# Performance work log

Hardware: AMD Instinct MI355X
Metric: run time of the kernel (lower is better)

## Reference

```python
import jax, jax.numpy as jnp
import numpy as np

B, S, HID, NH, HD = 2, 2048, 1024, 16, 64


def setup_inputs() -> dict:
    key = jax.random.key(0)
    k0, k1, k2, k3 = jax.random.split(key, 4)
    scale = 1.0 / np.sqrt(HID)
    return {
        "x": jax.random.normal(k0, (B, S, HID), dtype=jnp.float32),
        "wq": jax.random.normal(k1, (HID, HID), dtype=jnp.float32) * scale,
        "wk": jax.random.normal(k2, (HID, HID), dtype=jnp.float32) * scale,
        "wv": jax.random.normal(k3, (HID, HID), dtype=jnp.float32) * scale,
    }


def reference(x, wq, wk, wv):
    b, s, _ = x.shape
    # nn.Linear(bias=False): y = x @ W^T ; reshape to [B, H, S, D]
    q = (x @ wq.T).reshape(b, s, NH, HD).transpose(0, 2, 1, 3)
    k = (x @ wk.T).reshape(b, s, NH, HD).transpose(0, 2, 1, 3)
    v = (x @ wv.T).reshape(b, s, NH, HD).transpose(0, 2, 1, 3)
    att = jnp.einsum("bhqd,bhkd->bhqk", q, k) / np.sqrt(HD)
    score = jax.nn.softmax(att.astype(jnp.float32), axis=-1)  # dropout p=0.0 -> identity
    attv = jnp.einsum("bhqk,bhkd->bhqd", score, v)  # [B, H, S, D]
    # faithful to original bug: .view(B, S, -1) on contiguous [B,H,S,D] WITHOUT transpose back
    attv = attv.reshape(b, s, NH * HD)
    return score, attv
```

## Files before the change

### kernel.cpp

```cpp
#include <hip/hip_runtime.h>
#include <hip/hip_bf16.h>
#include <stdint.h>
#include <stddef.h>

#define NB 2
#define SEQ 2048
#define HIDN 1024
#define NHEAD 16
#define HDIM 64
#define MTOT (NB * SEQ)

typedef short bf16x8 __attribute__((ext_vector_type(8)));
typedef _Float16 f16x8 __attribute__((ext_vector_type(8)));
typedef __fp16 h16x2 __attribute__((ext_vector_type(2)));
typedef float f32x4 __attribute__((ext_vector_type(4)));
typedef uint32_t u32x4 __attribute__((ext_vector_type(4)));

#define MFMA16(a, b, c)  __builtin_amdgcn_mfma_f32_16x16x32_bf16(a, b, c, 0, 0, 0)
#define MFMAH16(a, b, c) __builtin_amdgcn_mfma_f32_16x16x32_f16(a, b, c, 0, 0, 0)

__device__ __forceinline__ unsigned short f2bf(float f) {
  union { float f; uint32_t u; } v; v.f = f;
  uint32_t u = v.u;
  uint32_t r = (u + 0x7fffu + ((u >> 16) & 1u)) >> 16;
  return (unsigned short)r;
}

__device__ __forceinline__ unsigned short f2h(float f) {
  _Float16 h = (_Float16)f;
  return *reinterpret_cast<unsigned short*>(&h);
}

__device__ __forceinline__ float h2f(unsigned short u) {
  _Float16 h = *reinterpret_cast<_Float16*>(&u);
  return (float)h;
}

__device__ __forceinline__ void gload16(const void* g, void* l) {
  __builtin_amdgcn_global_load_lds((const __attribute__((address_space(1))) void*)g,
                                   (__attribute__((address_space(3))) void*)l,
                                   16, 0, 0);
}

__global__ void cvt_bf16(const float* __restrict__ x, const float* __restrict__ wq,
                         const float* __restrict__ wk, const float* __restrict__ wv,
                         unsigned short* __restrict__ dst)
{
  size_t i4 = ((size_t)blockIdx.x * blockDim.x + threadIdx.x) * 4;
  const float* s; size_t off;
  if (i4 < 4194304UL)      { s = x;  off = i4; }
  else if (i4 < 5242880UL) { s = wq; off = i4 - 4194304UL; }
  else if (i4 < 6291456UL) { s = wk; off = i4 - 5242880UL; }
  else                     { s = wv; off = i4 - 6291456UL; }
  float4 v = *(const float4*)(s + off);
  ushort4 o;
  o.x = f2bf(v.x); o.y = f2bf(v.y); o.z = f2bf(v.z); o.w = f2bf(v.w);
  *(ushort4*)(dst + i4) = o;
}

__global__ __launch_bounds__(256, 2) void qkv_gemm(
    const unsigned short* __restrict__ xb,
    const unsigned short* __restrict__ wqb,
    const unsigned short* __restrict__ wkb,
    const unsigned short* __restrict__ wvb,
    unsigned short* __restrict__ Qb,
    unsigned short* __restrict__ Kb,
    unsigned short* __restrict__ Vt)
{
  __shared__ unsigned short As[128 * 64];
  __shared__ unsigned short Bs[128 * 64];

  const int z = blockIdx.z;
  const unsigned short* W = (z == 0) ? wqb : (z == 1) ? wkb : wvb;
  const int n0 = blockIdx.x * 128;
  const int m0 = blockIdx.y * 128;
  const int tid = threadIdx.x;
  const int lane = tid & 63;
  const int wid = tid >> 6;
  const int l15 = lane & 15;
  const int lg = lane >> 4;

  f32x4 acc[4][4] = {};

  const int wr = (wid >> 1) * 64;
  const int wc = (wid & 1) * 64;

  for (int kt = 0; kt < 16; ++kt) {
    __syncthreads();
    #pragma unroll
    for (int i = 0; i < 4; ++i) {
      int row = wid * 32 + i * 8 + (lane >> 3);
      int chunk = (lane & 7) ^ (row & 7);
      const unsigned short* ga = xb + (size_t)(m0 + row) * HIDN + kt * 64 + chunk * 8;
      const unsigned short* gb = W  + (size_t)(n0 + row) * HIDN + kt * 64 + chunk * 8;
      gload16(ga, (char*)As + wid * 4096 + i * 1024);
      gload16(gb, (char*)Bs + wid * 4096 + i * 1024);
    }
    __syncthreads();

    #pragma unroll
    for (int ks = 0; ks < 2; ++ks) {
      bf16x8 af[4], bfr[4];
      #pragma unroll
      for (int mi = 0; mi < 4; ++mi) {
        int row = wr + mi * 16 + l15;
        int cb = (ks * 64 + lg * 16) ^ ((row & 7) << 4);
        af[mi] = *(const bf16x8*)((const char*)As + row * 128 + cb);
      }
      #pragma unroll
      for (int ni = 0; ni < 4; ++ni) {
        int row = wc + ni * 16 + l15;
        int cb = (ks * 64 + lg * 16) ^ ((row & 7) << 4);
        bfr[ni] = *(const bf16x8*)((const char*)Bs + row * 128 + cb);
      }
      #pragma unroll
      for (int mi = 0; mi < 4; ++mi)
        #pragma unroll
        for (int ni = 0; ni < 4; ++ni)
          acc[mi][ni] = MFMA16(af[mi], bfr[ni], acc[mi][ni]);
    }
  }

  if (z < 2) {
    unsigned short* O = (z == 0) ? Qb : Kb;
    #pragma unroll
    for (int mi = 0; mi < 4; ++mi)
      #pragma unroll
      for (int ni = 0; ni < 4; ++ni) {
        int n = n0 + wc + ni * 16 + l15;
        #pragma unroll
        for (int e = 0; e < 4; ++e) {
          int m = m0 + wr + mi * 16 + lg * 4 + e;
          if (z == 0) {
            O[(size_t)m * HIDN + n] = f2bf(acc[mi][ni][e]);
          } else {
            int mm = (m & ~31) | (((m >> 2) & 1) << 4) | (((m >> 3) & 3) << 2) | (m & 3);
            int nn = (n & ~56) | (((((n >> 3) & 7) ^ (mm & 7))) << 3);
            O[(size_t)mm * HIDN + nn] = f2bf(acc[mi][ni][e]);
          }
        }
      }
  } else {
    #pragma unroll
    for (int mi = 0; mi < 4; ++mi)
      #pragma unroll
      for (int ni = 0; ni < 4; ++ni) {
        int n = n0 + wc + ni * 16 + l15;
        int m = m0 + wr + mi * 16 + lg * 4;
        int mmv = (m & ~120) | (((((m >> 3) & 15) ^ (n & 15))) << 3);
        ushort4 pk;
        pk.x = f2h(acc[mi][ni][0]);
        pk.y = f2h(acc[mi][ni][1]);
        pk.z = f2h(acc[mi][ni][2]);
        pk.w = f2h(acc[mi][ni][3]);
        *(ushort4*)(Vt + (size_t)n * MTOT + mmv) = pk;
      }
  }
}

__global__ __launch_bounds__(512, 4) void attn_pv(
    const unsigned short* __restrict__ Qb,
    const unsigned short* __restrict__ Kb,
    const unsigned short* __restrict__ Vt,
    float* __restrict__ invs,
    float* __restrict__ out)
{
  __shared__ unsigned short Ks[2][128 * 64];
  __shared__ unsigned short Vs[2][64 * 128];

  const int bid = blockIdx.x;
  const int xcd = bid & 7;
  const int rest = bid >> 3;
  const int pan = (rest & 3) * 8 + xcd;
  const int slab = rest >> 2;
  const int b = pan >> 4, h = pan & 15;
  const int tid = threadIdx.x;
  const int wid = tid >> 6;
  const int lane = tid & 63;
  const int l15 = lane & 15, lg = lane >> 4;
  const int q0 = slab * 128 + wid * 16;

  const unsigned short* qptr = Qb + ((size_t)(b * SEQ + q0 + l15) * HIDN + h * HDIM + lg * 8);
  const bf16x8 bq0 = *(const bf16x8*)qptr;
  const bf16x8 bq1 = *(const bf16x8*)(qptr + 32);

  const float C = 0.18033688011112042f;

  const unsigned short* kpanel = Kb + (size_t)b * SEQ * HIDN + h * HDIM;
  const unsigned short* vpanel = Vt + (size_t)h * HDIM * MTOT + b * SEQ;

  #define STAGE_K(buf, c) { \
    _Pragma("unroll") \
    for (int i = 0; i < 2; ++i) { \
      int row = wid * 8 + i * 64 + (lane >> 3); \
      const unsigned short* src = kpanel + (size_t)((c) * 128 + row) * HIDN + (lane & 7) * 8; \
      gload16(src, (char*)Ks[buf] + wid * 1024 + i * 8192); \
    } }
  #define STAGE_V(buf, c) { \
    _Pragma("unroll") \
    for (int i = 0; i < 2; ++i) { \
      int dl = wid * 4 + i * 32 + (lane >> 4); \
      const unsigned short* src = vpanel + (size_t)dl * MTOT + (c) * 128 + (lane & 15) * 8; \
      gload16(src, (char*)Vs[buf] + wid * 1024 + i * 8192); \
    } }

  STAGE_K(0, 0); STAGE_V(0, 0);
  __builtin_amdgcn_sched_barrier(0);
  asm volatile("s_waitcnt vmcnt(0)" ::: "memory");
  __builtin_amdgcn_s_barrier();
  __builtin_amdgcn_sched_barrier(0);

  float sm = 0.f;
  f32x4 pv[4] = {};

  for (int c = 0; c < 16; ++c) {
    const int cur = c & 1;
    if (c < 15) { STAGE_K(cur ^ 1, c + 1); STAGE_V(cur ^ 1, c + 1); }
    __builtin_amdgcn_sched_barrier(0);

    f32x4 acc[8] = {};
    #pragma unroll
    for (int kf = 0; kf < 8; ++kf) {
      const int rowL = kf * 16 + l15;
      const char* kr = (const char*)Ks[cur] + rowL * 128;
      bf16x8 a0 = *(const bf16x8*)(kr + ((lg    ) ^ (rowL & 7)) * 16);
      bf16x8 a1 = *(const bf16x8*)(kr + ((lg + 4) ^ (rowL & 7)) * 16);
      acc[kf] = MFMA16(a0, bq0, acc[kf]);
      acc[kf] = MFMA16(a1, bq1, acc[kf]);
    }

    #pragma unroll
    for (int t = 0; t < 4; ++t) {
      float4 s0, s1;
      s0.x = exp2f(acc[2 * t][0] * C);
      s0.y = exp2f(acc[2 * t][1] * C);
      s0.z = exp2f(acc[2 * t][2] * C);
      s0.w = exp2f(acc[2 * t][3] * C);
      s1.x = exp2f(acc[2 * t + 1][0] * C);
      s1.y = exp2f(acc[2 * t + 1][1] * C);
      s1.z = exp2f(acc[2 * t + 1][2] * C);
      s1.w = exp2f(acc[2 * t + 1][3] * C);
      sm += ((s0.x + s0.y) + (s0.z + s0.w)) + ((s1.x + s1.y) + (s1.z + s1.w));

      union PKu { h16x2 h2[4]; f16x8 h8; } pk;
      pk.h2[0] = __builtin_amdgcn_cvt_pkrtz(s0.x, s0.y);
      pk.h2[1] = __builtin_amdgcn_cvt_pkrtz(s0.z, s0.w);
      pk.h2[2] = __builtin_amdgcn_cvt_pkrtz(s1.x, s1.y);
      pk.h2[3] = __builtin_amdgcn_cvt_pkrtz(s1.z, s1.w);

      #pragma unroll
      for (int nf = 0; nf < 4; ++nf) {
        const int d = nf * 16 + l15;
        f16x8 bv = *(const f16x8*)((const char*)Vs[cur] + d * 256 + (((t * 4 + lg) ^ l15)) * 16);
        pv[nf] = MFMAH16(pk.h8, bv, pv[nf]);
      }
    }

    __builtin_amdgcn_sched_barrier(0);
    asm volatile("s_waitcnt vmcnt(0)" ::: "memory");
    __builtin_amdgcn_s_barrier();
    __builtin_amdgcn_sched_barrier(0);
  }

  #pragma unroll
  for (int off = 16; off <= 32; off <<= 1) sm += __shfl_xor(sm, off, 64);
  const float inv = __builtin_amdgcn_rcpf(sm);
  if (lane < 16) invs[(size_t)(b * NHEAD + h) * SEQ + q0 + lane] = inv;

  float* av = out + (size_t)NB * NHEAD * SEQ * SEQ
            + ((size_t)(b * NHEAD + h) * SEQ + q0 + 4 * lg) * HDIM + l15;
  #pragma unroll
  for (int e = 0; e < 4; ++e) {
    const float invq = __shfl(inv, 4 * lg + e, 64);
    #pragma unroll
    for (int nf = 0; nf < 4; ++nf)
      __builtin_nontemporal_store(pv[nf][e] * invq, av + (size_t)e * HDIM + nf * 16);
  }
  #undef STAGE_K
  #undef STAGE_V
}

__global__ __launch_bounds__(512, 2) void score_emit(
    const unsigned short* __restrict__ Qb,
    const unsigned short* __restrict__ Kb,
    const float* __restrict__ invs,
    float* __restrict__ out)
{
  __shared__ unsigned short P[16 * 2048];

  const int bid = blockIdx.x;
  const int xcd = bid & 7;
  const int rest = bid >> 3;
  const int pan = (rest & 3) * 8 + xcd;
  const int blkp = rest >> 2;
  const int b = pan >> 4, h = pan & 15;
  const int tid = threadIdx.x;
  const int wid = tid >> 6;
  const int lane = tid & 63;
  const int l15 = lane & 15, lg = lane >> 4;

  const float C = 0.18033688011112042f;
  const unsigned short* kpanel = Kb + (size_t)b * SEQ * HIDN + h * HDIM;
  const size_t panrow0 = (size_t)(b * NHEAD + h) * SEQ;

  for (int tt = 0; tt < 8; ++tt) {
    const int q0 = (blkp * 8 + tt) * 16;

    const unsigned short* qptr = Qb + ((size_t)(b * SEQ + q0 + l15) * HIDN + h * HDIM + lg * 8);
    const bf16x8 bq0 = *(const bf16x8*)qptr;
    const bf16x8 bq1 = *(const bf16x8*)(qptr + 32);

    #pragma unroll
    for (int i = 0; i < 2; ++i) {
      const int c = wid * 2 + i;
      f32x4 acc[8] = {};
      #pragma unroll
      for (int kf = 0; kf < 8; ++kf) {
        const int s = c * 128 + kf * 16 + l15;
        const unsigned short* kr = kpanel + (size_t)s * HIDN;
        bf16x8 a0 = *(const bf16x8*)(kr + ((lg      ^ (s & 7))) * 8);
        bf16x8 a1 = *(const bf16x8*)(kr + (((lg + 4) ^ (s & 7))) * 8);
        acc[kf] = MFMA16(a0, bq0, acc[kf]);
        acc[kf] = MFMA16(a1, bq1, acc[kf]);
      }
      #pragma unroll
      for (int t = 0; t < 4; ++t) {
        float4 s0, s1;
        s0.x = exp2f(acc[2 * t][0] * C);
        s0.y = exp2f(acc[2 * t][1] * C);
        s0.z = exp2f(acc[2 * t][2] * C);
        s0.w = exp2f(acc[2 * t][3] * C);
        s1.x = exp2f(acc[2 * t + 1][0] * C);
        s1.y = exp2f(acc[2 * t + 1][1] * C);
        s1.z = exp2f(acc[2 * t + 1][2] * C);
        s1.w = exp2f(acc[2 * t + 1][3] * C);

        union PKu { h16x2 h2[4]; u32x4 u4; } pk;
        pk.h2[0] = __builtin_amdgcn_cvt_pkrtz(s0.x, s0.y);
        pk.h2[1] = __builtin_amdgcn_cvt_pkrtz(s0.z, s0.w);
        pk.h2[2] = __builtin_amdgcn_cvt_pkrtz(s1.x, s1.y);
        pk.h2[3] = __builtin_amdgcn_cvt_pkrtz(s1.z, s1.w);

        const int off = c * 256 + ((((t * 4 + lg) ^ l15)) << 4);
        *(u32x4*)((char*)P + l15 * 4096 + off) = pk.u4;
      }
    }

    asm volatile("s_waitcnt lgkmcnt(0)" ::: "memory");
    __builtin_amdgcn_s_barrier();
    __builtin_amdgcn_sched_barrier(0);

    #pragma unroll
    for (int i = 0; i < 2; ++i) {
      const int r = wid * 2 + i;
      const float invr = invs[panrow0 + q0 + r];
      float* orow = out + (panrow0 + q0 + r) * SEQ;
      #pragma unroll
      for (int g = 0; g < 8; ++g) {
        const int o = g * 512 + lane * 8;
        const int ph = o ^ ((r & 15) << 4);
        uint2 w = *(const uint2*)((const char*)P + r * 4096 + ph);
        f32x4 ov;
        ov[0] = h2f((unsigned short)(w.x & 0xffff)) * invr;
        ov[1] = h2f((unsigned short)(w.x >> 16)) * invr;
        ov[2] = h2f((unsigned short)(w.y & 0xffff)) * invr;
        ov[3] = h2f((unsigned short)(w.y >> 16)) * invr;
        __builtin_nontemporal_store(ov, (f32x4*)(orow + (o >> 1)));
      }
    }

    asm volatile("s_waitcnt lgkmcnt(0)" ::: "memory");
    __builtin_amdgcn_s_barrier();
    __builtin_amdgcn_sched_barrier(0);
  }
}

extern "C" void kernel_launch(void* const* d_in, const int* in_sizes, int n_in,
                              void* d_out, int out_size, void* d_ws, size_t ws_size,
                              hipStream_t stream)
{
  const float* x  = (const float*)d_in[0];
  const float* wq = (const float*)d_in[1];
  const float* wk = (const float*)d_in[2];
  const float* wv = (const float*)d_in[3];
  float* out = (float*)d_out;
  unsigned short* ws = (unsigned short*)d_ws;

  unsigned short* xb  = ws;
  unsigned short* wqb = ws + 4194304;
  unsigned short* wkb = ws + 5242880;
  unsigned short* wvb = ws + 6291456;
  unsigned short* Qb  = ws + 7340032;
  unsigned short* Kb  = ws + 11534336;
  unsigned short* Vt  = ws + 15728640;
  float* invs = (float*)ws;

  cvt_bf16<<<7168, 256, 0, stream>>>(x, wq, wk, wv, ws);
  qkv_gemm<<<dim3(8, 32, 3), 256, 0, stream>>>(xb, wqb, wkb, wvb, Qb, Kb, Vt);
  attn_pv<<<512, 512, 0, stream>>>(Qb, Kb, Vt, invs, out);
  score_emit<<<512, 512, 0, stream>>>(Qb, Kb, invs, out);
}
```

Baseline: 195.0 us.

## Fuse PV attention and score emission into one kernel with per-tile row sums

Merges the two attention kernels into one. Each 16-row query tile computes QK^T exp values across all keys split over 8 waves, and reduces row sums through shared memory. It then writes normalized scores and computes P·V from register-held fp16 probabilities, followed by a cross-wave reduction of partial outputs in LDS. This removes the second QK^T recompute, the extra kernel launch and the invs round trip. In exchange it adds extra barriers, loads V directly from global without LDS staging, and adds an LDS reduction per tile.

```diff
diff --git a/kernel.cpp b/kernel.cpp
--- a/kernel.cpp
+++ b/kernel.cpp
@@ -158,135 +158,14 @@
   }
 }
 
-__global__ __launch_bounds__(512, 4) void attn_pv(
+__global__ __launch_bounds__(512, 2) void attn_all(
     const unsigned short* __restrict__ Qb,
     const unsigned short* __restrict__ Kb,
     const unsigned short* __restrict__ Vt,
-    float* __restrict__ invs,
-    float* __restrict__ out)
-{
-  __shared__ unsigned short Ks[2][128 * 64];
-  __shared__ unsigned short Vs[2][64 * 128];
-
-  const int bid = blockIdx.x;
-  const int xcd = bid & 7;
-  const int rest = bid >> 3;
-  const int pan = (rest & 3) * 8 + xcd;
-  const int slab = rest >> 2;
-  const int b = pan >> 4, h = pan & 15;
-  const int tid = threadIdx.x;
-  const int wid = tid >> 6;
-  const int lane = tid & 63;
-  const int l15 = lane & 15, lg = lane >> 4;
-  const int q0 = slab * 128 + wid * 16;
-
-  const unsigned short* qptr = Qb + ((size_t)(b * SEQ + q0 + l15) * HIDN + h * HDIM + lg * 8);
-  const bf16x8 bq0 = *(const bf16x8*)qptr;
-  const bf16x8 bq1 = *(const bf16x8*)(qptr + 32);
-
-  const float C = 0.18033688011112042f;
-
-  const unsigned short* kpanel = Kb + (size_t)b * SEQ * HIDN + h * HDIM;
-  const unsigned short* vpanel = Vt + (size_t)h * HDIM * MTOT + b * SEQ;
-
-  #define STAGE_K(buf, c) { \
-    _Pragma("unroll") \
-    for (int i = 0; i < 2; ++i) { \
-      int row = wid * 8 + i * 64 + (lane >> 3); \
-      const unsigned short* src = kpanel + (size_t)((c) * 128 + row) * HIDN + (lane & 7) * 8; \
-      gload16(src, (char*)Ks[buf] + wid * 1024 + i * 8192); \
-    } }
-  #define STAGE_V(buf, c) { \
-    _Pragma("unroll") \
-    for (int i = 0; i < 2; ++i) { \
-      int dl = wid * 4 + i * 32 + (lane >> 4); \
-      const unsigned short* src = vpanel + (size_t)dl * MTOT + (c) * 128 + (lane & 15) * 8; \
-      gload16(src, (char*)Vs[buf] + wid * 1024 + i * 8192); \
-    } }
-
-  STAGE_K(0, 0); STAGE_V(0, 0);
-  __builtin_amdgcn_sched_barrier(0);
-  asm volatile("s_waitcnt vmcnt(0)" ::: "memory");
-  __builtin_amdgcn_s_barrier();
-  __builtin_amdgcn_sched_barrier(0);
-
-  float sm = 0.f;
-  f32x4 pv[4] = {};
-
-  for (int c = 0; c < 16; ++c) {
-    const int cur = c & 1;
-    if (c < 15) { STAGE_K(cur ^ 1, c + 1); STAGE_V(cur ^ 1, c + 1); }
-    __builtin_amdgcn_sched_barrier(0);
-
-    f32x4 acc[8] = {};
-    #pragma unroll
-    for (int kf = 0; kf < 8; ++kf) {
-      const int rowL = kf * 16 + l15;
-      const char* kr = (const char*)Ks[cur] + rowL * 128;
-      bf16x8 a0 = *(const bf16x8*)(kr + ((lg    ) ^ (rowL & 7)) * 16);
-      bf16x8 a1 = *(const bf16x8*)(kr + ((lg + 4) ^ (rowL & 7)) * 16);
-      acc[kf] = MFMA16(a0, bq0, acc[kf]);
-      acc[kf] = MFMA16(a1, bq1, acc[kf]);
-    }
-
-    #pragma unroll
-    for (int t = 0; t < 4; ++t) {
-      float4 s0, s1;
-      s0.x = exp2f(acc[2 * t][0] * C);
-      s0.y = exp2f(acc[2 * t][1] * C);
-      s0.z = exp2f(acc[2 * t][2] * C);
-      s0.w = exp2f(acc[2 * t][3] * C);
-      s1.x = exp2f(acc[2 * t + 1][0] * C);
-      s1.y = exp2f(acc[2 * t + 1][1] * C);
-      s1.z = exp2f(acc[2 * t + 1][2] * C);
-      s1.w = exp2f(acc[2 * t + 1][3] * C);
-      sm += ((s0.x + s0.y) + (s0.z + s0.w)) + ((s1.x + s1.y) + (s1.z + s1.w));
-
-      union PKu { h16x2 h2[4]; f16x8 h8; } pk;
-      pk.h2[0] = __builtin_amdgcn_cvt_pkrtz(s0.x, s0.y);
-      pk.h2[1] = __builtin_amdgcn_cvt_pkrtz(s0.z, s0.w);
-      pk.h2[2] = __builtin_amdgcn_cvt_pkrtz(s1.x, s1.y);
-      pk.h2[3] = __builtin_amdgcn_cvt_pkrtz(s1.z, s1.w);
-
-      #pragma unroll
-      for (int nf = 0; nf < 4; ++nf) {
-        const int d = nf * 16 + l15;
-        f16x8 bv = *(const f16x8*)((const char*)Vs[cur] + d * 256 + (((t * 4 + lg) ^ l15)) * 16);
-        pv[nf] = MFMAH16(pk.h8, bv, pv[nf]);
-      }
-    }
-
-    __builtin_amdgcn_sched_barrier(0);
-    asm volatile("s_waitcnt vmcnt(0)" ::: "memory");
-    __builtin_amdgcn_s_barrier();
-    __builtin_amdgcn_sched_barrier(0);
-  }
-
-  #pragma unroll
-  for (int off = 16; off <= 32; off <<= 1) sm += __shfl_xor(sm, off, 64);
-  const float inv = __builtin_amdgcn_rcpf(sm);
-  if (lane < 16) invs[(size_t)(b * NHEAD + h) * SEQ + q0 + lane] = inv;
-
-  float* av = out + (size_t)NB * NHEAD * SEQ * SEQ
-            + ((size_t)(b * NHEAD + h) * SEQ + q0 + 4 * lg) * HDIM + l15;
-  #pragma unroll
-  for (int e = 0; e < 4; ++e) {
-    const float invq = __shfl(inv, 4 * lg + e, 64);
-    #pragma unroll
-    for (int nf = 0; nf < 4; ++nf)
-      __builtin_nontemporal_store(pv[nf][e] * invq, av + (size_t)e * HDIM + nf * 16);
-  }
-  #undef STAGE_K
-  #undef STAGE_V
-}
-
-__global__ __launch_bounds__(512, 2) void score_emit(
-    const unsigned short* __restrict__ Qb,
-    const unsigned short* __restrict__ Kb,
-    const float* __restrict__ invs,
     float* __restrict__ out)
 {
   __shared__ unsigned short P[16 * 2048];
+  __shared__ float sums[8][16];
 
   const int bid = blockIdx.x;
   const int xcd = bid & 7;
@@ -301,14 +180,20 @@
 
   const float C = 0.18033688011112042f;
   const unsigned short* kpanel = Kb + (size_t)b * SEQ * HIDN + h * HDIM;
+  const unsigned short* vpanel = Vt + (size_t)h * HDIM * MTOT + b * SEQ;
   const size_t panrow0 = (size_t)(b * NHEAD + h) * SEQ;
+  float* avbase = out + (size_t)NB * NHEAD * SEQ * SEQ;
 
   for (int tt = 0; tt < 8; ++tt) {
-    const int q0 = (blkp * 8 + tt) * 16;
+    const int q0 = blkp * 128 + tt * 16;
 
     const unsigned short* qptr = Qb + ((size_t)(b * SEQ + q0 + l15) * HIDN + h * HDIM + lg * 8);
     const bf16x8 bq0 = *(const bf16x8*)qptr;
     const bf16x8 bq1 = *(const bf16x8*)(qptr + 32);
+
+    union PKu { h16x2 h2[4]; f16x8 h8; u32x4 u4; };
+    u32x4 pkreg[2][4];
+    float sm = 0.f;
 
     #pragma unroll
     for (int i = 0; i < 2; ++i) {
@@ -334,39 +219,92 @@
         s1.y = exp2f(acc[2 * t + 1][1] * C);
         s1.z = exp2f(acc[2 * t + 1][2] * C);
         s1.w = exp2f(acc[2 * t + 1][3] * C);
-
-        union PKu { h16x2 h2[4]; u32x4 u4; } pk;
+        sm += ((s0.x + s0.y) + (s0.z + s0.w)) + ((s1.x + s1.y) + (s1.z + s1.w));
+
+        PKu pk;
         pk.h2[0] = __builtin_amdgcn_cvt_pkrtz(s0.x, s0.y);
         pk.h2[1] = __builtin_amdgcn_cvt_pkrtz(s0.z, s0.w);
         pk.h2[2] = __builtin_amdgcn_cvt_pkrtz(s1.x, s1.y);
         pk.h2[3] = __builtin_amdgcn_cvt_pkrtz(s1.z, s1.w);
+        pkreg[i][t] = pk.u4;
 
         const int off = c * 256 + ((((t * 4 + lg) ^ l15)) << 4);
         *(u32x4*)((char*)P + l15 * 4096 + off) = pk.u4;
       }
     }
+    sm += __shfl_xor(sm, 16, 64);
+    sm += __shfl_xor(sm, 32, 64);
+    if (lane < 16) sums[wid][lane] = sm;
 
     asm volatile("s_waitcnt lgkmcnt(0)" ::: "memory");
     __builtin_amdgcn_s_barrier();
     __builtin_amdgcn_sched_barrier(0);
 
+    float tot = 0.f;
+    #pragma unroll
+    for (int w2 = 0; w2 < 8; ++w2) tot += sums[w2][l15];
+    const float inv = __builtin_amdgcn_rcpf(tot);
+
+    f32x4 pv[4] = {};
+    #pragma unroll
+    for (int i = 0; i < 2; ++i) {
+      const int c = wid * 2 + i;
+      #pragma unroll
+      for (int t = 0; t < 4; ++t) {
+        PKu pk; pk.u4 = pkreg[i][t];
+        #pragma unroll
+        for (int nf = 0; nf < 4; ++nf) {
+          const unsigned short* vp = vpanel + (size_t)(nf * 16 + l15) * MTOT
+                                   + c * 128 + (((t * 4 + lg) ^ l15)) * 8;
+          f16x8 bv = *(const f16x8*)vp;
+          pv[nf] = MFMAH16(pk.h8, bv, pv[nf]);
+        }
+      }
+    }
+
     #pragma unroll
     for (int i = 0; i < 2; ++i) {
       const int r = wid * 2 + i;
-      const float invr = invs[panrow0 + q0 + r];
+      const float invr = __shfl(inv, r, 64);
       float* orow = out + (panrow0 + q0 + r) * SEQ;
       #pragma unroll
       for (int g = 0; g < 8; ++g) {
         const int o = g * 512 + lane * 8;
         const int ph = o ^ ((r & 15) << 4);
-        uint2 w = *(const uint2*)((const char*)P + r * 4096 + ph);
+        uint2 w2 = *(const uint2*)((const char*)P + r * 4096 + ph);
         f32x4 ov;
-        ov[0] = h2f((unsigned short)(w.x & 0xffff)) * invr;
-        ov[1] = h2f((unsigned short)(w.x >> 16)) * invr;
-        ov[2] = h2f((unsigned short)(w.y & 0xffff)) * invr;
-        ov[3] = h2f((unsigned short)(w.y >> 16)) * invr;
+        ov[0] = h2f((unsigned short)(w2.x & 0xffff)) * invr;
+        ov[1] = h2f((unsigned short)(w2.x >> 16)) * invr;
+        ov[2] = h2f((unsigned short)(w2.y & 0xffff)) * invr;
+        ov[3] = h2f((unsigned short)(w2.y >> 16)) * invr;
         __builtin_nontemporal_store(ov, (f32x4*)(orow + (o >> 1)));
       }
+    }
+
+    asm volatile("s_waitcnt lgkmcnt(0)" ::: "memory");
+    __builtin_amdgcn_s_barrier();
+    __builtin_amdgcn_sched_barrier(0);
+
+    float* pvred = (float*)P;
+    #pragma unroll
+    for (int nf = 0; nf < 4; ++nf)
+      #pragma unroll
+      for (int e = 0; e < 4; ++e)
+        pvred[(wid * 16 + (4 * lg + e)) * 68 + nf * 16 + l15] = pv[nf][e];
+
+    asm volatile("s_waitcnt lgkmcnt(0)" ::: "memory");
+    __builtin_amdgcn_s_barrier();
+    __builtin_amdgcn_sched_barrier(0);
+
+    #pragma unroll
+    for (int i = 0; i < 2; ++i) {
+      const int r = wid * 2 + i;
+      const float invr = __shfl(inv, r, 64);
+      float v = 0.f;
+      #pragma unroll
+      for (int w2 = 0; w2 < 8; ++w2)
+        v += pvred[(w2 * 16 + r) * 68 + lane];
+      __builtin_nontemporal_store(v * invr, avbase + (panrow0 + q0 + r) * HDIM + lane);
     }
 
     asm volatile("s_waitcnt lgkmcnt(0)" ::: "memory");
@@ -393,10 +331,8 @@
   unsigned short* Qb  = ws + 7340032;
   unsigned short* Kb  = ws + 11534336;
   unsigned short* Vt  = ws + 15728640;
-  float* invs = (float*)ws;
 
   cvt_bf16<<<7168, 256, 0, stream>>>(x, wq, wk, wv, ws);
   qkv_gemm<<<dim3(8, 32, 3), 256, 0, stream>>>(xb, wqb, wkb, wvb, Qb, Kb, Vt);
-  attn_pv<<<512, 512, 0, stream>>>(Qb, Kb, Vt, invs, out);
-  score_emit<<<512, 512, 0, stream>>>(Qb, Kb, invs, out);
-}
+  attn_all<<<512, 512, 0, stream>>>(Qb, Kb, Vt, out);
+}
```

Result: slower. 238.7 us (+22.4%).

## Double-buffer QKV GEMM LDS tiles and single-buffer K in attention for occupancy

Applied to the files above, without the earlier changes.

The QKV GEMM moves from a sync-load-sync loop to double-buffered LDS. The next k-tile's global-to-LDS copy is issued before computing on the current tile, so load latency overlaps MFMA work. The attention kernel drops K's second LDS buffer, adds a mid-iteration barrier so the next K chunk is loaded only after QK^T finishes, and raises the launch-bounds occupancy hint from 4 to 6. The trade is less LDS per block and more resident blocks, against an extra barrier and less overlap for K loads.

```diff
diff --git a/kernel.cpp b/kernel.cpp
--- a/kernel.cpp
+++ b/kernel.cpp
@@ -67,8 +67,8 @@
     unsigned short* __restrict__ Kb,
     unsigned short* __restrict__ Vt)
 {
-  __shared__ unsigned short As[128 * 64];
-  __shared__ unsigned short Bs[128 * 64];
+  __shared__ unsigned short As[2][128 * 64];
+  __shared__ unsigned short Bs[2][128 * 64];
 
   const int z = blockIdx.z;
   const unsigned short* W = (z == 0) ? wqb : (z == 1) ? wkb : wvb;
@@ -85,18 +85,27 @@
   const int wr = (wid >> 1) * 64;
   const int wc = (wid & 1) * 64;
 
+  #define QSTAGE(buf, kt) { \
+    _Pragma("unroll") \
+    for (int i = 0; i < 4; ++i) { \
+      int row = wid * 32 + i * 8 + (lane >> 3); \
+      int chunk = (lane & 7) ^ (row & 7); \
+      const unsigned short* ga = xb + (size_t)(m0 + row) * HIDN + (kt) * 64 + chunk * 8; \
+      const unsigned short* gb = W  + (size_t)(n0 + row) * HIDN + (kt) * 64 + chunk * 8; \
+      gload16(ga, (char*)As[buf] + wid * 4096 + i * 1024); \
+      gload16(gb, (char*)Bs[buf] + wid * 4096 + i * 1024); \
+    } }
+
+  QSTAGE(0, 0)
+  __builtin_amdgcn_sched_barrier(0);
+  asm volatile("s_waitcnt vmcnt(0) lgkmcnt(0)" ::: "memory");
+  __builtin_amdgcn_s_barrier();
+  __builtin_amdgcn_sched_barrier(0);
+
   for (int kt = 0; kt < 16; ++kt) {
-    __syncthreads();
-    #pragma unroll
-    for (int i = 0; i < 4; ++i) {
-      int row = wid * 32 + i * 8 + (lane >> 3);
-      int chunk = (lane & 7) ^ (row & 7);
-      const unsigned short* ga = xb + (size_t)(m0 + row) * HIDN + kt * 64 + chunk * 8;
-      const unsigned short* gb = W  + (size_t)(n0 + row) * HIDN + kt * 64 + chunk * 8;
-      gload16(ga, (char*)As + wid * 4096 + i * 1024);
-      gload16(gb, (char*)Bs + wid * 4096 + i * 1024);
-    }
-    __syncthreads();
+    const int cur = kt & 1;
+    if (kt < 15) QSTAGE(cur ^ 1, kt + 1)
+    __builtin_amdgcn_sched_barrier(0);
 
     #pragma unroll
     for (int ks = 0; ks < 2; ++ks) {
@@ -105,13 +114,13 @@
       for (int mi = 0; mi < 4; ++mi) {
         int row = wr + mi * 16 + l15;
         int cb = (ks * 64 + lg * 16) ^ ((row & 7) << 4);
-        af[mi] = *(const bf16x8*)((const char*)As + row * 128 + cb);
+        af[mi] = *(const bf16x8*)((const char*)As[cur] + row * 128 + cb);
       }
       #pragma unroll
       for (int ni = 0; ni < 4; ++ni) {
         int row = wc + ni * 16 + l15;
         int cb = (ks * 64 + lg * 16) ^ ((row & 7) << 4);
-        bfr[ni] = *(const bf16x8*)((const char*)Bs + row * 128 + cb);
+        bfr[ni] = *(const bf16x8*)((const char*)Bs[cur] + row * 128 + cb);
       }
       #pragma unroll
       for (int mi = 0; mi < 4; ++mi)
@@ -119,7 +128,13 @@
         for (int ni = 0; ni < 4; ++ni)
           acc[mi][ni] = MFMA16(af[mi], bfr[ni], acc[mi][ni]);
     }
+
+    __builtin_amdgcn_sched_barrier(0);
+    asm volatile("s_waitcnt vmcnt(0) lgkmcnt(0)" ::: "memory");
+    __builtin_amdgcn_s_barrier();
+    __builtin_amdgcn_sched_barrier(0);
   }
+  #undef QSTAGE
 
   if (z < 2) {
     unsigned short* O = (z == 0) ? Qb : Kb;
@@ -158,14 +173,14 @@
   }
 }
 
-__global__ __launch_bounds__(512, 4) void attn_pv(
+__global__ __launch_bounds__(512, 6) void attn_pv(
     const unsigned short* __restrict__ Qb,
     const unsigned short* __restrict__ Kb,
     const unsigned short* __restrict__ Vt,
     float* __restrict__ invs,
     float* __restrict__ out)
 {
-  __shared__ unsigned short Ks[2][128 * 64];
+  __shared__ unsigned short Ks[128 * 64];
   __shared__ unsigned short Vs[2][64 * 128];
 
   const int bid = blockIdx.x;
@@ -189,12 +204,12 @@
   const unsigned short* kpanel = Kb + (size_t)b * SEQ * HIDN + h * HDIM;
   const unsigned short* vpanel = Vt + (size_t)h * HDIM * MTOT + b * SEQ;
 
-  #define STAGE_K(buf, c) { \
+  #define STAGE_K(c) { \
     _Pragma("unroll") \
     for (int i = 0; i < 2; ++i) { \
       int row = wid * 8 + i * 64 + (lane >> 3); \
       const unsigned short* src = kpanel + (size_t)((c) * 128 + row) * HIDN + (lane & 7) * 8; \
-      gload16(src, (char*)Ks[buf] + wid * 1024 + i * 8192); \
+      gload16(src, (char*)Ks + wid * 1024 + i * 8192); \
     } }
   #define STAGE_V(buf, c) { \
     _Pragma("unroll") \
@@ -204,9 +219,9 @@
       gload16(src, (char*)Vs[buf] + wid * 1024 + i * 8192); \
     } }
 
-  STAGE_K(0, 0); STAGE_V(0, 0);
+  STAGE_K(0); STAGE_V(0, 0);
   __builtin_amdgcn_sched_barrier(0);
-  asm volatile("s_waitcnt vmcnt(0)" ::: "memory");
+  asm volatile("s_waitcnt vmcnt(0) lgkmcnt(0)" ::: "memory");
   __builtin_amdgcn_s_barrier();
   __builtin_amdgcn_sched_barrier(0);
 
@@ -215,19 +230,25 @@
 
   for (int c = 0; c < 16; ++c) {
     const int cur = c & 1;
-    if (c < 15) { STAGE_K(cur ^ 1, c + 1); STAGE_V(cur ^ 1, c + 1); }
-    __builtin_amdgcn_sched_barrier(0);
 
     f32x4 acc[8] = {};
     #pragma unroll
     for (int kf = 0; kf < 8; ++kf) {
       const int rowL = kf * 16 + l15;
-      const char* kr = (const char*)Ks[cur] + rowL * 128;
+      const char* kr = (const char*)Ks + rowL * 128;
       bf16x8 a0 = *(const bf16x8*)(kr + ((lg    ) ^ (rowL & 7)) * 16);
       bf16x8 a1 = *(const bf16x8*)(kr + ((lg + 4) ^ (rowL & 7)) * 16);
       acc[kf] = MFMA16(a0, bq0, acc[kf]);
       acc[kf] = MFMA16(a1, bq1, acc[kf]);
     }
+
+    __builtin_amdgcn_sched_barrier(0);
+    asm volatile("s_waitcnt lgkmcnt(0)" ::: "memory");
+    __builtin_amdgcn_s_barrier();
+    __builtin_amdgcn_sched_barrier(0);
+
+    if (c < 15) { STAGE_K(c + 1); STAGE_V(cur ^ 1, c + 1); }
+    __builtin_amdgcn_sched_barrier(0);
 
     #pragma unroll
     for (int t = 0; t < 4; ++t) {
@@ -257,7 +278,7 @@
     }
 
     __builtin_amdgcn_sched_barrier(0);
-    asm volatile("s_waitcnt vmcnt(0)" ::: "memory");
+    asm volatile("s_waitcnt vmcnt(0) lgkmcnt(0)" ::: "memory");
     __builtin_amdgcn_s_barrier();
     __builtin_amdgcn_sched_barrier(0);
   }
```

Measured after the change: 210.1 us. 1.08x slower.

## Merge attention-PV and score-emit kernels into one launch with independent row sums

Applied to the files above, without the earlier changes.

Combines the PV-accumulation kernel and the score-writing kernel into a single 1024-block launch. Even blocks do the PV path and odd blocks write the normalized score matrix. The score blocks now compute their own softmax row sums, reduced through shared memory, instead of reading inverse sums produced by the earlier kernel. This removes the dependency between the two kernels, so the compute-heavy PV blocks and the store-heavy score blocks can run concurrently. The cost is that the exp and QK^T work is done twice, and shared memory per block grows to the larger footprint, which may lower occupancy for the PV blocks.

```diff
diff --git a/kernel.cpp b/kernel.cpp
--- a/kernel.cpp
+++ b/kernel.cpp
@@ -158,171 +158,81 @@
   }
 }
 
-__global__ __launch_bounds__(512, 4) void attn_pv(
+__global__ __launch_bounds__(512, 2) void attn_split(
     const unsigned short* __restrict__ Qb,
     const unsigned short* __restrict__ Kb,
     const unsigned short* __restrict__ Vt,
-    float* __restrict__ invs,
     float* __restrict__ out)
 {
-  __shared__ unsigned short Ks[2][128 * 64];
-  __shared__ unsigned short Vs[2][64 * 128];
+  __shared__ char smem[66048];
 
   const int bid = blockIdx.x;
-  const int xcd = bid & 7;
-  const int rest = bid >> 3;
+  const int gg = bid >> 3;
+  const int type = gg & 1;
+  const int s = (bid & 7) | ((gg >> 1) << 3);
+
+  const int xcd = s & 7;
+  const int rest = s >> 3;
   const int pan = (rest & 3) * 8 + xcd;
-  const int slab = rest >> 2;
   const int b = pan >> 4, h = pan & 15;
   const int tid = threadIdx.x;
   const int wid = tid >> 6;
   const int lane = tid & 63;
   const int l15 = lane & 15, lg = lane >> 4;
-  const int q0 = slab * 128 + wid * 16;
-
-  const unsigned short* qptr = Qb + ((size_t)(b * SEQ + q0 + l15) * HIDN + h * HDIM + lg * 8);
-  const bf16x8 bq0 = *(const bf16x8*)qptr;
-  const bf16x8 bq1 = *(const bf16x8*)(qptr + 32);
 
   const float C = 0.18033688011112042f;
-
   const unsigned short* kpanel = Kb + (size_t)b * SEQ * HIDN + h * HDIM;
-  const unsigned short* vpanel = Vt + (size_t)h * HDIM * MTOT + b * SEQ;
-
-  #define STAGE_K(buf, c) { \
-    _Pragma("unroll") \
-    for (int i = 0; i < 2; ++i) { \
-      int row = wid * 8 + i * 64 + (lane >> 3); \
-      const unsigned short* src = kpanel + (size_t)((c) * 128 + row) * HIDN + (lane & 7) * 8; \
-      gload16(src, (char*)Ks[buf] + wid * 1024 + i * 8192); \
-    } }
-  #define STAGE_V(buf, c) { \
-    _Pragma("unroll") \
-    for (int i = 0; i < 2; ++i) { \
-      int dl = wid * 4 + i * 32 + (lane >> 4); \
-      const unsigned short* src = vpanel + (size_t)dl * MTOT + (c) * 128 + (lane & 15) * 8; \
-      gload16(src, (char*)Vs[buf] + wid * 1024 + i * 8192); \
-    } }
-
-  STAGE_K(0, 0); STAGE_V(0, 0);
-  __builtin_amdgcn_sched_barrier(0);
-  asm volatile("s_waitcnt vmcnt(0)" ::: "memory");
-  __builtin_amdgcn_s_barrier();
-  __builtin_amdgcn_sched_barrier(0);
-
-  float sm = 0.f;
-  f32x4 pv[4] = {};
-
-  for (int c = 0; c < 16; ++c) {
-    const int cur = c & 1;
-    if (c < 15) { STAGE_K(cur ^ 1, c + 1); STAGE_V(cur ^ 1, c + 1); }
-    __builtin_amdgcn_sched_barrier(0);
-
-    f32x4 acc[8] = {};
-    #pragma unroll
-    for (int kf = 0; kf < 8; ++kf) {
-      const int rowL = kf * 16 + l15;
-      const char* kr = (const char*)Ks[cur] + rowL * 128;
-      bf16x8 a0 = *(const bf16x8*)(kr + ((lg    ) ^ (rowL & 7)) * 16);
-      bf16x8 a1 = *(const bf16x8*)(kr + ((lg + 4) ^ (rowL & 7)) * 16);
-      acc[kf] = MFMA16(a0, bq0, acc[kf]);
-      acc[kf] = MFMA16(a1, bq1, acc[kf]);
-    }
-
-    #pragma unroll
-    for (int t = 0; t < 4; ++t) {
-      float4 s0, s1;
-      s0.x = exp2f(acc[2 * t][0] * C);
-      s0.y = exp2f(acc[2 * t][1] * C);
-      s0.z = exp2f(acc[2 * t][2] * C);
-      s0.w = exp2f(acc[2 * t][3] * C);
-      s1.x = exp2f(acc[2 * t + 1][0] * C);
-      s1.y = exp2f(acc[2 * t + 1][1] * C);
-      s1.z = exp2f(acc[2 * t + 1][2] * C);
-      s1.w = exp2f(acc[2 * t + 1][3] * C);
-      sm += ((s0.x + s0.y) + (s0.z + s0.w)) + ((s1.x + s1.y) + (s1.z + s1.w));
-
-      union PKu { h16x2 h2[4]; f16x8 h8; } pk;
-      pk.h2[0] = __builtin_amdgcn_cvt_pkrtz(s0.x, s0.y);
-      pk.h2[1] = __builtin_amdgcn_cvt_pkrtz(s0.z, s0.w);
-      pk.h2[2] = __builtin_amdgcn_cvt_pkrtz(s1.x, s1.y);
-      pk.h2[3] = __builtin_amdgcn_cvt_pkrtz(s1.z, s1.w);
-
-      #pragma unroll
-      for (int nf = 0; nf < 4; ++nf) {
-        const int d = nf * 16 + l15;
-        f16x8 bv = *(const f16x8*)((const char*)Vs[cur] + d * 256 + (((t * 4 + lg) ^ l15)) * 16);
-        pv[nf] = MFMAH16(pk.h8, bv, pv[nf]);
-      }
-    }
-
+  const size_t panrow0 = (size_t)(b * NHEAD + h) * SEQ;
+
+  if (type == 0) {
+    const int slab = rest >> 2;
+    const int q0 = slab * 128 + wid * 16;
+
+    const unsigned short* qptr = Qb + ((size_t)(b * SEQ + q0 + l15) * HIDN + h * HDIM + lg * 8);
+    const bf16x8 bq0 = *(const bf16x8*)qptr;
+    const bf16x8 bq1 = *(const bf16x8*)(qptr + 32);
+    const unsigned short* vpanel = Vt + (size_t)h * HDIM * MTOT + b * SEQ;
+
+    #define STAGE_K(buf, c) { \
+      _Pragma("unroll") \
+      for (int i = 0; i < 2; ++i) { \
+        int row = wid * 8 + i * 64 + (lane >> 3); \
+        const unsigned short* src = kpanel + (size_t)((c) * 128 + row) * HIDN + (lane & 7) * 8; \
+        gload16(src, smem + (buf) * 16384 + wid * 1024 + i * 8192); \
+      } }
+    #define STAGE_V(buf, c) { \
+      _Pragma("unroll") \
+      for (int i = 0; i < 2; ++i) { \
+        int dl = wid * 4 + i * 32 + (lane >> 4); \
+        const unsigned short* src = vpanel + (size_t)dl * MTOT + (c) * 128 + (lane & 15) * 8; \
+        gload16(src, smem + 32768 + (buf) * 16384 + wid * 1024 + i * 8192); \
+      } }
+
+    STAGE_K(0, 0); STAGE_V(0, 0);
     __builtin_amdgcn_sched_barrier(0);
     asm volatile("s_waitcnt vmcnt(0)" ::: "memory");
     __builtin_amdgcn_s_barrier();
     __builtin_amdgcn_sched_barrier(0);
-  }
-
-  #pragma unroll
-  for (int off = 16; off <= 32; off <<= 1) sm += __shfl_xor(sm, off, 64);
-  const float inv = __builtin_amdgcn_rcpf(sm);
-  if (lane < 16) invs[(size_t)(b * NHEAD + h) * SEQ + q0 + lane] = inv;
-
-  float* av = out + (size_t)NB * NHEAD * SEQ * SEQ
-            + ((size_t)(b * NHEAD + h) * SEQ + q0 + 4 * lg) * HDIM + l15;
-  #pragma unroll
-  for (int e = 0; e < 4; ++e) {
-    const float invq = __shfl(inv, 4 * lg + e, 64);
-    #pragma unroll
-    for (int nf = 0; nf < 4; ++nf)
-      __builtin_nontemporal_store(pv[nf][e] * invq, av + (size_t)e * HDIM + nf * 16);
-  }
-  #undef STAGE_K
-  #undef STAGE_V
-}
-
-__global__ __launch_bounds__(512, 2) void score_emit(
-    const unsigned short* __restrict__ Qb,
-    const unsigned short* __restrict__ Kb,
-    const float* __restrict__ invs,
-    float* __restrict__ out)
-{
-  __shared__ unsigned short P[16 * 2048];
-
-  const int bid = blockIdx.x;
-  const int xcd = bid & 7;
-  const int rest = bid >> 3;
-  const int pan = (rest & 3) * 8 + xcd;
-  const int blkp = rest >> 2;
-  const int b = pan >> 4, h = pan & 15;
-  const int tid = threadIdx.x;
-  const int wid = tid >> 6;
-  const int lane = tid & 63;
-  const int l15 = lane & 15, lg = lane >> 4;
-
-  const float C = 0.18033688011112042f;
-  const unsigned short* kpanel = Kb + (size_t)b * SEQ * HIDN + h * HDIM;
-  const size_t panrow0 = (size_t)(b * NHEAD + h) * SEQ;
-
-  for (int tt = 0; tt < 8; ++tt) {
-    const int q0 = (blkp * 8 + tt) * 16;
-
-    const unsigned short* qptr = Qb + ((size_t)(b * SEQ + q0 + l15) * HIDN + h * HDIM + lg * 8);
-    const bf16x8 bq0 = *(const bf16x8*)qptr;
-    const bf16x8 bq1 = *(const bf16x8*)(qptr + 32);
-
-    #pragma unroll
-    for (int i = 0; i < 2; ++i) {
-      const int c = wid * 2 + i;
+
+    float sm = 0.f;
+    f32x4 pv[4] = {};
+
+    for (int c = 0; c < 16; ++c) {
+      const int cur = c & 1;
+      if (c < 15) { STAGE_K(cur ^ 1, c + 1); STAGE_V(cur ^ 1, c + 1); }
+      __builtin_amdgcn_sched_barrier(0);
+
       f32x4 acc[8] = {};
       #pragma unroll
       for (int kf = 0; kf < 8; ++kf) {
-        const int s = c * 128 + kf * 16 + l15;
-        const unsigned short* kr = kpanel + (size_t)s * HIDN;
-        bf16x8 a0 = *(const bf16x8*)(kr + ((lg      ^ (s & 7))) * 8);
-        bf16x8 a1 = *(const bf16x8*)(kr + (((lg + 4) ^ (s & 7))) * 8);
+        const int rowL = kf * 16 + l15;
+        const char* kr = smem + cur * 16384 + rowL * 128;
+        bf16x8 a0 = *(const bf16x8*)(kr + ((lg    ) ^ (rowL & 7)) * 16);
+        bf16x8 a1 = *(const bf16x8*)(kr + ((lg + 4) ^ (rowL & 7)) * 16);
         acc[kf] = MFMA16(a0, bq0, acc[kf]);
         acc[kf] = MFMA16(a1, bq1, acc[kf]);
       }
+
       #pragma unroll
       for (int t = 0; t < 4; ++t) {
         float4 s0, s1;
@@ -334,44 +244,129 @@
         s1.y = exp2f(acc[2 * t + 1][1] * C);
         s1.z = exp2f(acc[2 * t + 1][2] * C);
         s1.w = exp2f(acc[2 * t + 1][3] * C);
-
-        union PKu { h16x2 h2[4]; u32x4 u4; } pk;
+        sm += ((s0.x + s0.y) + (s0.z + s0.w)) + ((s1.x + s1.y) + (s1.z + s1.w));
+
+        union PKu { h16x2 h2[4]; f16x8 h8; } pk;
         pk.h2[0] = __builtin_amdgcn_cvt_pkrtz(s0.x, s0.y);
         pk.h2[1] = __builtin_amdgcn_cvt_pkrtz(s0.z, s0.w);
         pk.h2[2] = __builtin_amdgcn_cvt_pkrtz(s1.x, s1.y);
         pk.h2[3] = __builtin_amdgcn_cvt_pkrtz(s1.z, s1.w);
 
-        const int off = c * 256 + ((((t * 4 + lg) ^ l15)) << 4);
-        *(u32x4*)((char*)P + l15 * 4096 + off) = pk.u4;
-      }
-    }
-
-    asm volatile("s_waitcnt lgkmcnt(0)" ::: "memory");
-    __builtin_amdgcn_s_barrier();
-    __builtin_amdgcn_sched_barrier(0);
-
-    #pragma unroll
-    for (int i = 0; i < 2; ++i) {
-      const int r = wid * 2 + i;
-      const float invr = invs[panrow0 + q0 + r];
-      float* orow = out + (panrow0 + q0 + r) * SEQ;
-      #pragma unroll
-      for (int g = 0; g < 8; ++g) {
-        const int o = g * 512 + lane * 8;
-        const int ph = o ^ ((r & 15) << 4);
-        uint2 w = *(const uint2*)((const char*)P + r * 4096 + ph);
-        f32x4 ov;
-        ov[0] = h2f((unsigned short)(w.x & 0xffff)) * invr;
-        ov[1] = h2f((unsigned short)(w.x >> 16)) * invr;
-        ov[2] = h2f((unsigned short)(w.y & 0xffff)) * invr;
-        ov[3] = h2f((unsigned short)(w.y >> 16)) * invr;
-        __builtin_nontemporal_store(ov, (f32x4*)(orow + (o >> 1)));
-      }
-    }
-
-    asm volatile("s_waitcnt lgkmcnt(0)" ::: "memory");
-    __builtin_amdgcn_s_barrier();
-    __builtin_amdgcn_sched_barrier(0);
+        #pragma unroll
+        for (int nf = 0; nf < 4; ++nf) {
+          const int d = nf * 16 + l15;
+          f16x8 bv = *(const f16x8*)(smem + 32768 + cur * 16384 + d * 256 + (((t * 4 + lg) ^ l15)) * 16);
+          pv[nf] = MFMAH16(pk.h8, bv, pv[nf]);
+        }
+      }
+
+      __builtin_amdgcn_sched_barrier(0);
+      asm volatile("s_waitcnt vmcnt(0)" ::: "memory");
+      __builtin_amdgcn_s_barrier();
+      __builtin_amdgcn_sched_barrier(0);
+    }
+
+    #pragma unroll
+    for (int off = 16; off <= 32; off <<= 1) sm += __shfl_xor(sm, off, 64);
+    const float inv = __builtin_amdgcn_rcpf(sm);
+
+    float* av = out + (size_t)NB * NHEAD * SEQ * SEQ
+              + (panrow0 + q0 + 4 * lg) * HDIM + l15;
+    #pragma unroll
+    for (int e = 0; e < 4; ++e) {
+      const float invq = __shfl(inv, 4 * lg + e, 64);
+      #pragma unroll
+      for (int nf = 0; nf < 4; ++nf)
+        __builtin_nontemporal_store(pv[nf][e] * invq, av + (size_t)e * HDIM + nf * 16);
+    }
+    #undef STAGE_K
+    #undef STAGE_V
+
+  } else {
+    unsigned short* P = (unsigned short*)smem;
+    float* sums = (float*)(smem + 65536);
+    const int blkp = rest >> 2;
+
+    for (int tt = 0; tt < 8; ++tt) {
+      const int q0 = (blkp * 8 + tt) * 16;
+
+      const unsigned short* qptr = Qb + ((size_t)(b * SEQ + q0 + l15) * HIDN + h * HDIM + lg * 8);
+      const bf16x8 bq0 = *(const bf16x8*)qptr;
+      const bf16x8 bq1 = *(const bf16x8*)(qptr + 32);
+
+      float sm = 0.f;
+      #pragma unroll
+      for (int i = 0; i < 2; ++i) {
+        const int c = wid * 2 + i;
+        f32x4 acc[8] = {};
+        #pragma unroll
+        for (int kf = 0; kf < 8; ++kf) {
+          const int sr = c * 128 + kf * 16 + l15;
+          const unsigned short* kr = kpanel + (size_t)sr * HIDN;
+          bf16x8 a0 = *(const bf16x8*)(kr + ((lg      ^ (sr & 7))) * 8);
+          bf16x8 a1 = *(const bf16x8*)(kr + (((lg + 4) ^ (sr & 7))) * 8);
+          acc[kf] = MFMA16(a0, bq0, acc[kf]);
+          acc[kf] = MFMA16(a1, bq1, acc[kf]);
+        }
+        #pragma unroll
+        for (int t = 0; t < 4; ++t) {
+          float4 s0, s1;
+          s0.x = exp2f(acc[2 * t][0] * C);
+          s0.y = exp2f(acc[2 * t][1] * C);
+          s0.z = exp2f(acc[2 * t][2] * C);
+          s0.w = exp2f(acc[2 * t][3] * C);
+          s1.x = exp2f(acc[2 * t + 1][0] * C);
+          s1.y = exp2f(acc[2 * t + 1][1] * C);
+          s1.z = exp2f(acc[2 * t + 1][2] * C);
+          s1.w = exp2f(acc[2 * t + 1][3] * C);
+          sm += ((s0.x + s0.y) + (s0.z + s0.w)) + ((s1.x + s1.y) + (s1.z + s1.w));
+
+          union PKu { h16x2 h2[4]; u32x4 u4; } pk;
+          pk.h2[0] = __builtin_amdgcn_cvt_pkrtz(s0.x, s0.y);
+          pk.h2[1] = __builtin_amdgcn_cvt_pkrtz(s0.z, s0.w);
+          pk.h2[2] = __builtin_amdgcn_cvt_pkrtz(s1.x, s1.y);
+          pk.h2[3] = __builtin_amdgcn_cvt_pkrtz(s1.z, s1.w);
+
+          const int off = c * 256 + ((((t * 4 + lg) ^ l15)) << 4);
+          *(u32x4*)((char*)P + l15 * 4096 + off) = pk.u4;
+        }
+      }
+      sm += __shfl_xor(sm, 16, 64);
+      sm += __shfl_xor(sm, 32, 64);
+      if (lane < 16) sums[wid * 16 + lane] = sm;
+
+      asm volatile("s_waitcnt lgkmcnt(0)" ::: "memory");
+      __builtin_amdgcn_s_barrier();
+      __builtin_amdgcn_sched_barrier(0);
+
+      float tot = 0.f;
+      #pragma unroll
+      for (int w2 = 0; w2 < 8; ++w2) tot += sums[w2 * 16 + l15];
+      const float inv = __builtin_amdgcn_rcpf(tot);
+
+      #pragma unroll
+      for (int i = 0; i < 2; ++i) {
+        const int r = wid * 2 + i;
+        const float invr = __shfl(inv, r, 64);
+        float* orow = out + (panrow0 + q0 + r) * SEQ;
+        #pragma unroll
+        for (int g = 0; g < 8; ++g) {
+          const int o = g * 512 + lane * 8;
+          const int ph = o ^ ((r & 15) << 4);
+          uint2 w = *(const uint2*)((const char*)P + r * 4096 + ph);
+          f32x4 ov;
+          ov[0] = h2f((unsigned short)(w.x & 0xffff)) * invr;
+          ov[1] = h2f((unsigned short)(w.x >> 16)) * invr;
+          ov[2] = h2f((unsigned short)(w.y & 0xffff)) * invr;
+          ov[3] = h2f((unsigned short)(w.y >> 16)) * invr;
+          __builtin_nontemporal_store(ov, (f32x4*)(orow + (o >> 1)));
+        }
+      }
+
+      asm volatile("s_waitcnt lgkmcnt(0)" ::: "memory");
+      __builtin_amdgcn_s_barrier();
+      __builtin_amdgcn_sched_barrier(0);
+    }
   }
 }
 
@@ -393,10 +388,8 @@
   unsigned short* Qb  = ws + 7340032;
   unsigned short* Kb  = ws + 11534336;
   unsigned short* Vt  = ws + 15728640;
-  float* invs = (float*)ws;
 
   cvt_bf16<<<7168, 256, 0, stream>>>(x, wq, wk, wv, ws);
   qkv_gemm<<<dim3(8, 32, 3), 256, 0, stream>>>(xb, wqb, wkb, wvb, Qb, Kb, Vt);
-  attn_pv<<<512, 512, 0, stream>>>(Qb, Kb, Vt, invs, out);
-  score_emit<<<512, 512, 0, stream>>>(Qb, Kb, invs, out);
-}
+  attn_split<<<1024, 512, 0, stream>>>(Qb, Kb, Vt, out);
+}
```

Result: slower. 199.9 us (+2.5%).
